# Performance work log

Hardware: AMD Instinct MI355X
Metric: run time of the kernel (lower is better)

Reference implementation:

```python
import jax, jax.numpy as jnp
import numpy as np
from jax import lax

K = 3  # dynamic/static conv kernel size
C = 64  # n_feat (hard-coded by Linear(64, ...) in the module)


def leaky(x):
    return jax.nn.leaky_relu(x, 0.1)


def conv2d(x, w, b, pad):
    # x: [B,C,H,W], w: [O,I,kh,kw] (OIHW), b: [O]
    y = lax.conv_general_dilated(x, w, (1, 1), [(pad, pad), (pad, pad)],
                                 dimension_numbers=("NCHW", "OIHW", "NCHW"))
    return y + b.reshape(1, -1, 1, 1)


def rda_conv(x, d, k1, k2, cw, cb):
    # x: [B,C,H,W], d: [B,64]
    b, c, h, w = x.shape
    hid = leaky(d @ k1)                        # [B,64]
    kern = (hid @ k2).reshape(b * c, 1, K, K)  # per-(batch,channel) kernel
    pad = (K - 1) // 2
    # depthwise dynamic conv: groups = b*c
    out = lax.conv_general_dilated(x.reshape(1, b * c, h, w), kern, (1, 1),
                                   [(pad, pad), (pad, pad)],
                                   feature_group_count=b * c,
                                   dimension_numbers=("NCHW", "OIHW", "NCHW"))
    out = leaky(out).reshape(b, c, h, w)
    M = jax.nn.sigmoid(conv2d(x, cw, cb, 0))   # [B,1,H,W] gating map
    return out * M + x


def setup_inputs() -> dict:
    key = jax.random.key(0)
    ks = jax.random.split(key, 14)
    s = 0.05
    inp = {
        "x": jax.random.normal(ks[0], (16, C, 128, 128), jnp.float32),
        "d": jax.random.normal(ks[1], (16, C), jnp.float32),
        # RDA_conv 1: kernel MLP (stored as [in,out]) + 1x1 gating conv
        "da1_k1": jax.random.normal(ks[2], (64, 64), jnp.float32) * s,
        "da1_k2": jax.random.normal(ks[3], (64, 64 * K * K), jnp.float32) * s,
        "da1_cw": jax.random.normal(ks[4], (1, C, 1, 1), jnp.float32) * s,
        "da1_cb": jax.random.normal(ks[5], (1,), jnp.float32) * s,
        # RDA_conv 2
        "da2_k1": jax.random.normal(ks[6], (64, 64), jnp.float32) * s,
        "da2_k2": jax.random.normal(ks[7], (64, 64 * K * K), jnp.float32) * s,
        "da2_cw": jax.random.normal(ks[8], (1, C, 1, 1), jnp.float32) * s,
        "da2_cb": jax.random.normal(ks[9], (1,), jnp.float32) * s,
        # static 3x3 convs
        "conv1_w": jax.random.normal(ks[10], (C, C, K, K), jnp.float32) * s,
        "conv1_b": jax.random.normal(ks[11], (C,), jnp.float32) * s,
        "conv2_w": jax.random.normal(ks[12], (C, C, K, K), jnp.float32) * s,
        "conv2_b": jax.random.normal(ks[13], (C,), jnp.float32) * s,
    }
    return inp


def reference(x, d, da1_k1, da1_k2, da1_cw, da1_cb, da2_k1, da2_k2, da2_cw,
              da2_cb, conv1_w, conv1_b, conv2_w, conv2_b):
    pad = (K - 1) // 2
    out = leaky(rda_conv(x, d, da1_k1, da1_k2, da1_cw, da1_cb))
    out = leaky(conv2d(out, conv1_w, conv1_b, pad))
    out = leaky(rda_conv(out, d, da2_k1, da2_k2, da2_cw, da2_cb))
    out = conv2d(out, conv2_w, conv2_b, pad) + x
    return out
```

## Files before the change

### kernel.cpp

```cpp
#include <hip/hip_runtime.h>
#include <hip/hip_bf16.h>
#include <math.h>

#define B_ 16
#define C_ 64
#define H_ 128
#define W_ 128
#define HW_ (H_*W_)
#define CHW_ (C_*HW_)
#define NTOT_ (B_*CHW_)

typedef __attribute__((ext_vector_type(8))) short short8;
typedef __attribute__((ext_vector_type(4))) float float4v;

__device__ __forceinline__ float leaky(float v) { return v > 0.f ? v : 0.1f * v; }
__device__ __forceinline__ float b2f(__hip_bfloat16 h) { return __bfloat162float(h); }

__global__ __launch_bounds__(192) void k_dyn(
    const float* __restrict__ d,
    const float* __restrict__ k1a, const float* __restrict__ k2a,
    const float* __restrict__ k1b, const float* __restrict__ k2b,
    float* __restrict__ kernA, float* __restrict__ kernB)
{
    const int which = blockIdx.x / 48;
    const int r     = blockIdx.x % 48;
    const int b     = r / 3;
    const int chunk = r % 3;
    const float* k1 = which ? k1b : k1a;
    const float* k2 = which ? k2b : k2a;
    float* outp = which ? kernB : kernA;

    __shared__ float hid[64];
    const int tid = threadIdx.x;
    if (tid < 64) {
        float s = 0.f;
        #pragma unroll
        for (int i = 0; i < 64; ++i) s = fmaf(d[b*64 + i], k1[i*64 + tid], s);
        hid[tid] = leaky(s);
    }
    __syncthreads();
    const int o = chunk * 192 + tid;
    float s = 0.f;
    #pragma unroll
    for (int j = 0; j < 64; ++j) s = fmaf(hid[j], k2[j*576 + o], s);
    outp[b*576 + (o % 9)*64 + (o / 9)] = s;
}

__global__ void k_prepw(const float* __restrict__ W1, const float* __restrict__ W2,
                        __hip_bfloat16* __restrict__ P1, __hip_bfloat16* __restrict__ P2)
{
    const int s = blockIdx.x;
    const int which = blockIdx.y;
    const float* W = which ? W2 : W1;
    __hip_bfloat16* P = which ? P2 : P1;
    const int t = s >> 1, half = s & 1;
    for (int idx = threadIdx.x; idx < 2048; idx += 256) {
        const int oc = idx >> 5, kk = idx & 31;
        P[s*2048 + idx] = __float2bfloat16(W[oc*576 + (half*32 + kk)*9 + t]);
    }
}

__global__ __launch_bounds__(256) void k_pre(const float* __restrict__ X,
                                             const float* __restrict__ cw,
                                             const float* __restrict__ cb,
                                             __hip_bfloat16* __restrict__ Xn,
                                             float* __restrict__ G1)
{
    __shared__ float sT[64][65];
    __shared__ float pG[4][64];
    const int b = blockIdx.y;
    const int p0 = blockIdx.x * 64;
    const int tid = threadIdx.x;
    #pragma unroll
    for (int i = 0; i < 16; ++i) {
        int idx = i*256 + tid;
        int c = idx >> 6, p = idx & 63;
        sT[c][p] = X[(size_t)b*CHW_ + (size_t)c*HW_ + p0 + p];
    }
    __syncthreads();
    #pragma unroll
    for (int i = 0; i < 16; ++i) {
        int idx = i*256 + tid;
        int p = idx >> 6, c = idx & 63;
        Xn[((size_t)b*HW_ + p0 + p)*64 + c] = __float2bfloat16(sT[c][p]);
    }
    const int cg = tid >> 6, p = tid & 63;
    float part = 0.f;
    #pragma unroll
    for (int c = 0; c < 16; ++c) part = fmaf(sT[cg*16 + c][p], cw[cg*16 + c], part);
    pG[cg][p] = part;
    __syncthreads();
    if (tid < 64) {
        float g = pG[0][tid] + pG[1][tid] + pG[2][tid] + pG[3][tid] + cb[0];
        G1[(size_t)b*HW_ + p0 + tid] = 1.f / (1.f + __expf(-g));
    }
}

__global__ __launch_bounds__(256) void k_rda_nhwc(
    const __hip_bfloat16* __restrict__ Xn, const float* __restrict__ kernN,
    const float* __restrict__ G, __hip_bfloat16* __restrict__ Out)
{
    const int lane = threadIdx.x & 63;
    const int wv = threadIdx.x >> 6;
    const int gid = blockIdx.x * 4 + wv;
    const int b = gid >> 11;
    const int rem = gid & 2047;
    const int h = rem >> 4;
    const int w0 = (rem & 15) * 8;

    float k9[9];
    #pragma unroll
    for (int t = 0; t < 9; ++t) k9[t] = kernN[((size_t)b*9 + t)*64 + lane];

    const __hip_bfloat16* Xb = Xn + (size_t)b * HW_ * 64 + lane;
    float r[3][10];
    #pragma unroll
    for (int dh = 0; dh < 3; ++dh) {
        const int hh = h - 1 + dh;
        if ((unsigned)hh < (unsigned)H_) {
            const __hip_bfloat16* rp = Xb + ((size_t)hh*W_ + w0) * 64;
            r[dh][0] = (w0 > 0) ? b2f(rp[-64]) : 0.f;
            #pragma unroll
            for (int j = 1; j < 9; ++j) r[dh][j] = b2f(rp[(j-1)*64]);
            r[dh][9] = (w0 + 8 < W_) ? b2f(rp[8*64]) : 0.f;
        } else {
            #pragma unroll
            for (int j = 0; j < 10; ++j) r[dh][j] = 0.f;
        }
    }

    const float* Gp = G + (size_t)b*HW_ + (size_t)h*W_ + w0;
    __hip_bfloat16* Op = Out + ((size_t)b*HW_ + (size_t)h*W_ + w0)*64 + lane;
    #pragma unroll
    for (int i = 0; i < 8; ++i) {
        float s = 0.f;
        #pragma unroll
        for (int dh = 0; dh < 3; ++dh)
            #pragma unroll
            for (int dw = 0; dw < 3; ++dw)
                s = fmaf(r[dh][i + dw], k9[dh*3 + dw], s);
        const float xc = r[1][i + 1];
        const float m = Gp[i];
        Op[i*64] = __float2bfloat16(leaky(leaky(s)*m + xc));
    }
}

template<int MODE>
__global__ __launch_bounds__(256) void k_conv_mfma(
    const __hip_bfloat16* __restrict__ Xn, const __hip_bfloat16* __restrict__ Wpk,
    const float* __restrict__ bias, const float* __restrict__ Xres,
    const float* __restrict__ Gcw, const float* __restrict__ Gcb,
    __hip_bfloat16* __restrict__ OutN, float* __restrict__ OutF,
    float* __restrict__ G2)
{
    __shared__ short sA[18*18*64];
    const int tid = threadIdx.x;
    const int b = blockIdx.y;
    const int h0 = (blockIdx.x >> 3) * 16;
    const int w0 = (blockIdx.x & 7) * 16;

    const short* Xs = (const short*)Xn;
    for (int idx = tid; idx < 2592; idx += 256) {
        const int cc = idx & 7;
        const int w = (idx >> 3) % 18;
        const int r = idx / 144;
        const int gh = h0 - 1 + r;
        const int gw = w0 - 1 + w;
        uint4 v = make_uint4(0, 0, 0, 0);
        if ((unsigned)gh < (unsigned)H_ && (unsigned)gw < (unsigned)W_)
            v = *(const uint4*)(Xs + (((size_t)b*H_ + gh)*W_ + gw)*64 + cc*8);
        *(uint4*)(sA + ((r*18 + w)*64 + ((cc ^ (w & 7)) * 8))) = v;
    }
    __syncthreads();

    const int lane = tid & 63;
    const int wv = tid >> 6;
    const int l15 = lane & 15;
    const int lq = lane >> 4;

    float4v acc[4][4];
    #pragma unroll
    for (int i = 0; i < 4; ++i)
        #pragma unroll
        for (int j = 0; j < 4; ++j) acc[i][j] = (float4v)0.f;

    const short* Wp = (const short*)Wpk;

    #pragma unroll
    for (int s = 0; s < 18; ++s) {
        const int t = s >> 1, half = s & 1;
        const int dh = t / 3, dwx = t % 3;
        short8 afr[4], bfr[4];
        #pragma unroll
        for (int mt = 0; mt < 4; ++mt) {
            const int r = wv*4 + mt + dh;
            const int w = l15 + dwx;
            const int chunk = (half*4 + lq) ^ (w & 7);
            afr[mt] = *(const short8*)(sA + ((r*18 + w)*64 + chunk*8));
        }
        #pragma unroll
        for (int nt = 0; nt < 4; ++nt)
            bfr[nt] = *(const short8*)(Wp + ((size_t)s*2048 + (nt*16 + l15)*32 + lq*8));
        #pragma unroll
        for (int mt = 0; mt < 4; ++mt)
            #pragma unroll
            for (int nt = 0; nt < 4; ++nt)
                acc[mt][nt] = __builtin_amdgcn_mfma_f32_16x16x32_bf16(
                    afr[mt], bfr[nt], acc[mt][nt], 0, 0, 0);
    }

    float bs[4], cwv[4], cbv = 0.f;
    #pragma unroll
    for (int nt = 0; nt < 4; ++nt) bs[nt] = bias[nt*16 + l15];
    if (MODE == 0) {
        #pragma unroll
        for (int nt = 0; nt < 4; ++nt) cwv[nt] = Gcw[nt*16 + l15];
        cbv = Gcb[0];
    }

    #pragma unroll
    for (int mt = 0; mt < 4; ++mt) {
        const int pr = wv*4 + mt;
        if (MODE == 0) {
            float vv[4][4];
            #pragma unroll
            for (int nt = 0; nt < 4; ++nt)
                #pragma unroll
                for (int rg = 0; rg < 4; ++rg)
                    vv[nt][rg] = leaky(acc[mt][nt][rg] + bs[nt]);
            #pragma unroll
            for (int nt = 0; nt < 4; ++nt) {
                const int n = nt*16 + l15;
                #pragma unroll
                for (int rg = 0; rg < 4; ++rg) {
                    const int pw = lq*4 + rg;
                    OutN[(((size_t)b*H_ + h0 + pr)*W_ + w0 + pw)*64 + n] =
                        __float2bfloat16(vv[nt][rg]);
                }
            }
            #pragma unroll
            for (int rg = 0; rg < 4; ++rg) {
                float p = vv[0][rg]*cwv[0] + vv[1][rg]*cwv[1]
                        + vv[2][rg]*cwv[2] + vv[3][rg]*cwv[3];
                p += __shfl_xor(p, 1);
                p += __shfl_xor(p, 2);
                p += __shfl_xor(p, 4);
                p += __shfl_xor(p, 8);
                if (l15 == 0)
                    G2[(size_t)b*HW_ + (size_t)(h0 + pr)*W_ + w0 + lq*4 + rg] =
                        1.f / (1.f + __expf(-(p + cbv)));
            }
        } else {
            #pragma unroll
            for (int nt = 0; nt < 4; ++nt) {
                const int n = nt*16 + l15;
                const size_t base = ((size_t)(b*64 + n)*H_ + h0 + pr)*W_ + w0 + lq*4;
                const float4 xr = *(const float4*)(Xres + base);
                float4 v;
                v.x = acc[mt][nt][0] + bs[nt] + xr.x;
                v.y = acc[mt][nt][1] + bs[nt] + xr.y;
                v.z = acc[mt][nt][2] + bs[nt] + xr.z;
                v.w = acc[mt][nt][3] + bs[nt] + xr.w;
                *(float4*)(OutF + base) = v;
            }
        }
    }
}

extern "C" void kernel_launch(void* const* d_in, const int* in_sizes, int n_in,
                              void* d_out, int out_size, void* d_ws, size_t ws_size,
                              hipStream_t stream)
{
    const float* x       = (const float*)d_in[0];
    const float* d       = (const float*)d_in[1];
    const float* da1_k1  = (const float*)d_in[2];
    const float* da1_k2  = (const float*)d_in[3];
    const float* da1_cw  = (const float*)d_in[4];
    const float* da1_cb  = (const float*)d_in[5];
    const float* da2_k1  = (const float*)d_in[6];
    const float* da2_k2  = (const float*)d_in[7];
    const float* da2_cw  = (const float*)d_in[8];
    const float* da2_cb  = (const float*)d_in[9];
    const float* conv1_w = (const float*)d_in[10];
    const float* conv1_b = (const float*)d_in[11];
    const float* conv2_w = (const float*)d_in[12];
    const float* conv2_b = (const float*)d_in[13];
    float* out = (float*)d_out;

    __hip_bfloat16* bufA = (__hip_bfloat16*)d_ws;
    __hip_bfloat16* bufB = bufA + NTOT_;
    float* kernA = (float*)(bufB + NTOT_);
    float* kernB = kernA + 16*576;
    __hip_bfloat16* wpk1 = (__hip_bfloat16*)(kernB + 16*576);
    __hip_bfloat16* wpk2 = wpk1 + 18*64*32;
    float* G1 = (float*)(wpk2 + 18*64*32);
    float* G2 = G1 + (size_t)B_*HW_;

    k_dyn<<<dim3(96), dim3(192), 0, stream>>>(d, da1_k1, da1_k2, da2_k1, da2_k2,
                                              kernA, kernB);
    k_prepw<<<dim3(18, 2), dim3(256), 0, stream>>>(conv1_w, conv2_w, wpk1, wpk2);
    k_pre<<<dim3(HW_/64, B_), dim3(256), 0, stream>>>(x, da1_cw, da1_cb, bufA, G1);
    k_rda_nhwc<<<dim3(B_*HW_/32), dim3(256), 0, stream>>>(bufA, kernA, G1, bufB);
    k_conv_mfma<0><<<dim3(64, B_), dim3(256), 0, stream>>>(
        bufB, wpk1, conv1_b, nullptr, da2_cw, da2_cb, bufA, nullptr, G2);
    k_rda_nhwc<<<dim3(B_*HW_/32), dim3(256), 0, stream>>>(bufA, kernB, G2, bufB);
    k_conv_mfma<1><<<dim3(64, B_), dim3(256), 0, stream>>>(
        bufB, wpk2, conv2_b, x, nullptr, nullptr, nullptr, out, nullptr);
}
```

Before: 278.8 us.

## Fuse dynamic depthwise RDA conv into the MFMA 3x3 conv kernel via LDS halo

```diff
diff --git a/kernel.cpp b/kernel.cpp
--- a/kernel.cpp
+++ b/kernel.cpp
@@ -14,7 +14,13 @@
 typedef __attribute__((ext_vector_type(4))) float float4v;
 
 __device__ __forceinline__ float leaky(float v) { return v > 0.f ? v : 0.1f * v; }
-__device__ __forceinline__ float b2f(__hip_bfloat16 h) { return __bfloat162float(h); }
+__device__ __forceinline__ float bs2f(short u) {
+    return __uint_as_float(((unsigned)(unsigned short)u) << 16);
+}
+__device__ __forceinline__ short f2bs(float v) {
+    __hip_bfloat16 h = __float2bfloat16(v);
+    union { __hip_bfloat16 h; short s; } u; u.h = h; return u.s;
+}
 
 __global__ __launch_bounds__(192) void k_dyn(
     const float* __restrict__ d,
@@ -53,10 +59,10 @@
     const int which = blockIdx.y;
     const float* W = which ? W2 : W1;
     __hip_bfloat16* P = which ? P2 : P1;
-    const int t = s >> 1, half = s & 1;
+    const int t = s >> 1, hf = s & 1;
     for (int idx = threadIdx.x; idx < 2048; idx += 256) {
         const int oc = idx >> 5, kk = idx & 31;
-        P[s*2048 + idx] = __float2bfloat16(W[oc*576 + (half*32 + kk)*9 + t]);
+        P[s*2048 + idx] = __float2bfloat16(W[oc*576 + (hf*32 + kk)*9 + t]);
     }
 }
 
@@ -96,85 +102,102 @@
     }
 }
 
-__global__ __launch_bounds__(256) void k_rda_nhwc(
+template<int MODE>
+__global__ __launch_bounds__(256) void k_rda_conv(
     const __hip_bfloat16* __restrict__ Xn, const float* __restrict__ kernN,
-    const float* __restrict__ G, __hip_bfloat16* __restrict__ Out)
-{
-    const int lane = threadIdx.x & 63;
-    const int wv = threadIdx.x >> 6;
-    const int gid = blockIdx.x * 4 + wv;
-    const int b = gid >> 11;
-    const int rem = gid & 2047;
-    const int h = rem >> 4;
-    const int w0 = (rem & 15) * 8;
-
-    float k9[9];
-    #pragma unroll
-    for (int t = 0; t < 9; ++t) k9[t] = kernN[((size_t)b*9 + t)*64 + lane];
-
-    const __hip_bfloat16* Xb = Xn + (size_t)b * HW_ * 64 + lane;
-    float r[3][10];
-    #pragma unroll
-    for (int dh = 0; dh < 3; ++dh) {
-        const int hh = h - 1 + dh;
-        if ((unsigned)hh < (unsigned)H_) {
-            const __hip_bfloat16* rp = Xb + ((size_t)hh*W_ + w0) * 64;
-            r[dh][0] = (w0 > 0) ? b2f(rp[-64]) : 0.f;
-            #pragma unroll
-            for (int j = 1; j < 9; ++j) r[dh][j] = b2f(rp[(j-1)*64]);
-            r[dh][9] = (w0 + 8 < W_) ? b2f(rp[8*64]) : 0.f;
-        } else {
-            #pragma unroll
-            for (int j = 0; j < 10; ++j) r[dh][j] = 0.f;
-        }
-    }
-
-    const float* Gp = G + (size_t)b*HW_ + (size_t)h*W_ + w0;
-    __hip_bfloat16* Op = Out + ((size_t)b*HW_ + (size_t)h*W_ + w0)*64 + lane;
-    #pragma unroll
-    for (int i = 0; i < 8; ++i) {
-        float s = 0.f;
-        #pragma unroll
-        for (int dh = 0; dh < 3; ++dh)
-            #pragma unroll
-            for (int dw = 0; dw < 3; ++dw)
-                s = fmaf(r[dh][i + dw], k9[dh*3 + dw], s);
-        const float xc = r[1][i + 1];
-        const float m = Gp[i];
-        Op[i*64] = __float2bfloat16(leaky(leaky(s)*m + xc));
-    }
-}
-
-template<int MODE>
-__global__ __launch_bounds__(256) void k_conv_mfma(
-    const __hip_bfloat16* __restrict__ Xn, const __hip_bfloat16* __restrict__ Wpk,
+    const float* __restrict__ G, const __hip_bfloat16* __restrict__ Wpk,
     const float* __restrict__ bias, const float* __restrict__ Xres,
     const float* __restrict__ Gcw, const float* __restrict__ Gcb,
     __hip_bfloat16* __restrict__ OutN, float* __restrict__ OutF,
     float* __restrict__ G2)
 {
-    __shared__ short sA[18*18*64];
+    __shared__ short sA[20*20*64];
     const int tid = threadIdx.x;
     const int b = blockIdx.y;
     const int h0 = (blockIdx.x >> 3) * 16;
     const int w0 = (blockIdx.x & 7) * 16;
+    const int lane = tid & 63;
+    const int wv = tid >> 6;
 
     const short* Xs = (const short*)Xn;
-    for (int idx = tid; idx < 2592; idx += 256) {
+    for (int idx = tid; idx < 3200; idx += 256) {
         const int cc = idx & 7;
-        const int w = (idx >> 3) % 18;
-        const int r = idx / 144;
-        const int gh = h0 - 1 + r;
-        const int gw = w0 - 1 + w;
+        const int w = (idx >> 3) % 20;
+        const int r = idx / 160;
+        const int gh = h0 - 2 + r;
+        const int gw = w0 - 2 + w;
         uint4 v = make_uint4(0, 0, 0, 0);
         if ((unsigned)gh < (unsigned)H_ && (unsigned)gw < (unsigned)W_)
             v = *(const uint4*)(Xs + (((size_t)b*H_ + gh)*W_ + gw)*64 + cc*8);
-        *(uint4*)(sA + ((r*18 + w)*64 + ((cc ^ (w & 7)) * 8))) = v;
-    }
+        *(uint4*)(sA + ((r*20 + w)*64 + ((cc ^ (w & 7)) * 8))) = v;
+    }
+
+    float k9[9];
+    #pragma unroll
+    for (int t = 0; t < 9; ++t) k9[t] = kernN[((size_t)b*9 + t)*64 + lane];
+
+    int loff[8];
+    #pragma unroll
+    for (int jc = 0; jc < 8; ++jc)
+        loff[jc] = (((lane >> 3) ^ jc) << 3) + (lane & 7);
+
     __syncthreads();
 
-    const int lane = tid & 63;
-    const int wv = tid >> 6;
+    for (int round = 0; round < 5; ++round) {
+        const int r = round*4 + wv;
+        const bool active = (r < 18);
+        float outv[18];
+        if (active) {
+            const int gh = h0 - 1 + r;
+            if ((unsigned)gh < (unsigned)H_) {
+                #pragma unroll
+                for (int w = 0; w < 18; ++w) outv[w] = 0.f;
+                const float* Gp = G + (size_t)b*HW_ + (size_t)gh*W_ + (w0 - 1);
+                const short* r0 = sA + (r*20)*64;
+                const short* r1 = r0 + 20*64;
+                const short* r2 = r1 + 20*64;
+                float c1p = 0.f;
+                #pragma unroll
+                for (int j = 0; j < 20; ++j) {
+                    const int off = j*64 + loff[j & 7];
+                    const float c0 = bs2f(r0[off]);
+                    const float c1 = bs2f(r1[off]);
+                    const float c2 = bs2f(r2[off]);
+                    #pragma unroll
+                    for (int dw = 0; dw < 3; ++dw) {
+                        const int w = j - dw;
+                        if (w >= 0 && w < 18)
+                            outv[w] = fmaf(c0, k9[dw],
+                                      fmaf(c1, k9[3+dw],
+                                      fmaf(c2, k9[6+dw], outv[w])));
+                    }
+                    const int wf = j - 2;
+                    if (wf >= 0) {
+                        const int gw = w0 - 1 + wf;
+                        float val = 0.f;
+                        if ((unsigned)gw < (unsigned)W_) {
+                            const float m = Gp[wf];
+                            val = leaky(leaky(outv[wf]) * m + c1p);
+                        }
+                        outv[wf] = val;
+                    }
+                    c1p = c1;
+                }
+            } else {
+                #pragma unroll
+                for (int w = 0; w < 18; ++w) outv[w] = 0.f;
+            }
+        }
+        __syncthreads();
+        if (active) {
+            short* wp = sA + (r*20)*64;
+            #pragma unroll
+            for (int w = 0; w < 18; ++w)
+                wp[w*64 + loff[w & 7]] = f2bs(outv[w]);
+        }
+        __syncthreads();
+    }
+
     const int l15 = lane & 15;
     const int lq = lane >> 4;
 
@@ -188,15 +211,15 @@
 
     #pragma unroll
     for (int s = 0; s < 18; ++s) {
-        const int t = s >> 1, half = s & 1;
+        const int t = s >> 1, hf = s & 1;
         const int dh = t / 3, dwx = t % 3;
         short8 afr[4], bfr[4];
         #pragma unroll
         for (int mt = 0; mt < 4; ++mt) {
             const int r = wv*4 + mt + dh;
             const int w = l15 + dwx;
-            const int chunk = (half*4 + lq) ^ (w & 7);
-            afr[mt] = *(const short8*)(sA + ((r*18 + w)*64 + chunk*8));
+            const int chunk = (hf*4 + lq) ^ (w & 7);
+            afr[mt] = *(const short8*)(sA + ((r*20 + w)*64 + chunk*8));
         }
         #pragma unroll
         for (int nt = 0; nt < 4; ++nt)
@@ -300,10 +323,8 @@
                                               kernA, kernB);
     k_prepw<<<dim3(18, 2), dim3(256), 0, stream>>>(conv1_w, conv2_w, wpk1, wpk2);
     k_pre<<<dim3(HW_/64, B_), dim3(256), 0, stream>>>(x, da1_cw, da1_cb, bufA, G1);
-    k_rda_nhwc<<<dim3(B_*HW_/32), dim3(256), 0, stream>>>(bufA, kernA, G1, bufB);
-    k_conv_mfma<0><<<dim3(64, B_), dim3(256), 0, stream>>>(
-        bufB, wpk1, conv1_b, nullptr, da2_cw, da2_cb, bufA, nullptr, G2);
-    k_rda_nhwc<<<dim3(B_*HW_/32), dim3(256), 0, stream>>>(bufA, kernB, G2, bufB);
-    k_conv_mfma<1><<<dim3(64, B_), dim3(256), 0, stream>>>(
-        bufB, wpk2, conv2_b, x, nullptr, nullptr, nullptr, out, nullptr);
-}
+    k_rda_conv<0><<<dim3(64, B_), dim3(256), 0, stream>>>(
+        bufA, kernA, G1, wpk1, conv1_b, nullptr, da2_cw, da2_cb, bufB, nullptr, G2);
+    k_rda_conv<1><<<dim3(64, B_), dim3(256), 0, stream>>>(
+        bufB, kernB, G2, wpk2, conv2_b, x, nullptr, nullptr, nullptr, out, nullptr);
+}
```

After: 259.5 us. 1.07x faster.
